# Performance work log

Hardware: AMD Instinct MI355X
Metric: run time of the kernel (lower is better)

## Reference

```python
import jax, jax.numpy as jnp
import numpy as np


def setup_inputs() -> dict:
    key = jax.random.key(0)
    ks = jax.random.split(key, 6)
    B, S, D, L = 4, 4096, 1024, 8192
    return {
        "inputs": jax.random.normal(ks[0], (B, S, D), dtype=jnp.float32),
        "W_w": jax.random.normal(ks[1], (D, D), dtype=jnp.float32) * (1.0 / np.sqrt(D)),
        "W_b": jax.random.normal(ks[2], (D,), dtype=jnp.float32) * 0.02,
        "U_w": jax.random.normal(ks[3], (L, D), dtype=jnp.float32) * (1.0 / np.sqrt(D)),
        "final_w": jax.random.normal(ks[4], (L, D), dtype=jnp.float32) * (1.0 / np.sqrt(D)),
        "final_b": jax.random.normal(ks[5], (L,), dtype=jnp.float32) * 0.02,
    }


def reference(inputs, W_w, W_b, U_w, final_w, final_b):
    # Z = tanh(W(inputs)): [B,S,D]
    Z = jnp.tanh(jnp.einsum("bsd,ed->bse", inputs, W_w) + W_b)
    # scores = U.weight @ Z^T: [B,L,S], softmax over seq
    scores = jnp.einsum("ld,bsd->bls", U_w, Z)
    alpha = jax.nn.softmax(scores, axis=2)
    # hidden = alpha @ inputs: [B,L,D]
    hidden = jnp.einsum("bls,bsd->bld", alpha, inputs)
    # logits = sum_d final_w[l,d]*hidden[b,l,d] + final_b[l]: [B,L]
    logits = jnp.einsum("ld,bld->bl", final_w, hidden) + final_b
    return logits
```

## Files before the change

### kernel.cpp

```cpp
#include <hip/hip_runtime.h>

typedef __attribute__((ext_vector_type(8))) short bf16x8;
typedef __attribute__((ext_vector_type(4))) float f32x4;

#define DEVINL __device__ __forceinline__
#define AS1 __attribute__((address_space(1)))
#define AS3 __attribute__((address_space(3)))

constexpr int BB = 4, SS = 4096, DD = 1024, LL = 8192;
constexpr int LT = 128, ST = 128, BK = 64, NS = 2;
constexpr int NL = LL / LT;
constexpr int SCHUNK = SS / NS;
constexpr int NST = SCHUNK / ST;
constexpr int KST = DD / BK;
constexpr int TILE = LT * BK;

DEVINL unsigned short f2bf(float f){
  union { float f; unsigned u; } a; a.f = f;
  unsigned r = a.u + 0x7fffu + ((a.u >> 16) & 1u);
  return (unsigned short)(r >> 16);
}

DEVINL void gll16(const void* src, void* dst){
  __builtin_amdgcn_global_load_lds((const AS1 unsigned int*)src,
                                   (AS3 unsigned int*)dst, 16, 0, 0);
}

DEVINL void stage_tile(const unsigned short* __restrict__ g0, int row0, int d0,
                       unsigned short* ldsbase, int wave, int lane){
#pragma unroll
  for (int it = 0; it < 4; ++it){
    int off  = it*4096 + wave*1024 + lane*16;
    int row  = off >> 7;
    int slot = (off >> 4) & 7;
    int scol = (slot ^ (row & 7)) << 3;
    gll16(g0 + (size_t)(row0 + row) * DD + d0 + scol,
          ldsbase + ((it*4096 + wave*1024) >> 1));
  }
}

DEVINL bf16x8 read_frag(const unsigned short* tile, int row, int chunk){
  return *(const AS3 bf16x8*)(tile + row*BK + ((chunk ^ (row & 7)) << 3));
}

__global__ void conv_kernel(const float4* __restrict__ in,
                            ushort4* __restrict__ out, int n4){
  int stride = gridDim.x * blockDim.x;
  for (int i = blockIdx.x*blockDim.x + threadIdx.x; i < n4; i += stride){
    float4 v = in[i];
    ushort4 o;
    o.x = f2bf(v.x); o.y = f2bf(v.y); o.z = f2bf(v.z); o.w = f2bf(v.w);
    out[i] = o;
  }
}

__global__ __launch_bounds__(256, 2) void zgemm_kernel(
    const unsigned short* __restrict__ X, const unsigned short* __restrict__ W,
    const float* __restrict__ Wb, unsigned short* __restrict__ Z)
{
  __shared__ __align__(16) unsigned short lds[2*TILE];
  const int bid = blockIdx.x;
  const int tm = bid & 127;
  const int tn = bid >> 7;
  const int tid = threadIdx.x, wave = tid >> 6, lane = tid & 63;
  const int wl = wave >> 1, wn = wave & 1;
  const int g = lane >> 4, cc = lane & 15;

  f32x4 acc[4][4] = {};
#pragma unroll 1
  for (int ks = 0; ks < KST; ++ks){
    __syncthreads();
    stage_tile(X, tm*LT, ks*BK, lds,        wave, lane);
    stage_tile(W, tn*LT, ks*BK, lds + TILE, wave, lane);
    __syncthreads();
#pragma unroll
    for (int ksub = 0; ksub < 2; ++ksub){
      bf16x8 af[4], bfr[4];
#pragma unroll
      for (int f = 0; f < 4; ++f) af[f]  = read_frag(lds,        wl*64 + f*16 + cc, ksub*4 + g);
#pragma unroll
      for (int f = 0; f < 4; ++f) bfr[f] = read_frag(lds + TILE, wn*64 + f*16 + cc, ksub*4 + g);
#pragma unroll
      for (int fm = 0; fm < 4; ++fm)
#pragma unroll
        for (int fn = 0; fn < 4; ++fn)
          acc[fm][fn] = __builtin_amdgcn_mfma_f32_16x16x32_bf16(af[fm], bfr[fn], acc[fm][fn], 0, 0, 0);
    }
  }
#pragma unroll
  for (int fm = 0; fm < 4; ++fm)
#pragma unroll
    for (int fn = 0; fn < 4; ++fn)
#pragma unroll
      for (int r = 0; r < 4; ++r){
        int row = tm*LT + wl*64 + fm*16 + 4*g + r;
        int col = tn*LT + wn*64 + fn*16 + cc;
        float y = acc[fm][fn][r] + Wb[col];
        float e2 = __expf(2.f * y);
        float t = 1.f - 2.f / (e2 + 1.f);
        Z[(size_t)row*DD + col] = f2bf(t);
      }
}

__global__ __launch_bounds__(256, 2) void fused_kernel(
    const unsigned short* __restrict__ U, const unsigned short* __restrict__ F,
    const unsigned short* __restrict__ Z, const unsigned short* __restrict__ X,
    float* __restrict__ pse, float* __restrict__ pac)
{
  __shared__ __align__(16) unsigned short lds[4*TILE];
  const int h = blockIdx.x;
  const int logical = (h & 7) * 64 + (h >> 3);
  const int lt  = logical & (NL - 1);
  const int grp = logical >> 6;
  const int sp  = grp & (NS - 1);
  const int b   = grp >> 1;

  const int tid = threadIdx.x, wave = tid >> 6, lane = tid & 63;
  const int wl = wave >> 1, wsc = wave & 1;
  const int g = lane >> 4, cc = lane & 15;

  const unsigned short* Ub = U + (size_t)lt*LT*DD;
  const unsigned short* Fb = F + (size_t)lt*LT*DD;
  const unsigned short* Zb = Z + ((size_t)b*SS + (size_t)sp*SCHUNK) * DD;
  const unsigned short* Xb = X + ((size_t)b*SS + (size_t)sp*SCHUNK) * DD;

  float se_st[4][4] = {}, ac_st[4][4] = {};

#pragma unroll 1
  for (int st = 0; st < NST; ++st){
    f32x4 sacc[4][4] = {}, gacc[4][4] = {};
#pragma unroll 1
    for (int ks = 0; ks < KST; ++ks){
      __syncthreads();
      stage_tile(Ub, 0,     ks*BK, lds,          wave, lane);
      stage_tile(Fb, 0,     ks*BK, lds +   TILE, wave, lane);
      stage_tile(Zb, st*ST, ks*BK, lds + 2*TILE, wave, lane);
      stage_tile(Xb, st*ST, ks*BK, lds + 3*TILE, wave, lane);
      __syncthreads();
#pragma unroll
      for (int ksub = 0; ksub < 2; ++ksub){
        bf16x8 a0[4], b0[4];
#pragma unroll
        for (int f = 0; f < 4; ++f) a0[f] = read_frag(lds,          wl*64  + f*16 + cc, ksub*4 + g);
#pragma unroll
        for (int f = 0; f < 4; ++f) b0[f] = read_frag(lds + 2*TILE, wsc*64 + f*16 + cc, ksub*4 + g);
#pragma unroll
        for (int fm = 0; fm < 4; ++fm)
#pragma unroll
          for (int fn = 0; fn < 4; ++fn)
            sacc[fm][fn] = __builtin_amdgcn_mfma_f32_16x16x32_bf16(a0[fm], b0[fn], sacc[fm][fn], 0, 0, 0);
#pragma unroll
        for (int f = 0; f < 4; ++f) a0[f] = read_frag(lds +   TILE, wl*64  + f*16 + cc, ksub*4 + g);
#pragma unroll
        for (int f = 0; f < 4; ++f) b0[f] = read_frag(lds + 3*TILE, wsc*64 + f*16 + cc, ksub*4 + g);
#pragma unroll
        for (int fm = 0; fm < 4; ++fm)
#pragma unroll
          for (int fn = 0; fn < 4; ++fn)
            gacc[fm][fn] = __builtin_amdgcn_mfma_f32_16x16x32_bf16(a0[fm], b0[fn], gacc[fm][fn], 0, 0, 0);
      }
    }
#pragma unroll
    for (int fm = 0; fm < 4; ++fm)
#pragma unroll
      for (int r = 0; r < 4; ++r){
        float ps = 0.f, pg = 0.f;
#pragma unroll
        for (int fn = 0; fn < 4; ++fn){
          float p = __expf(sacc[fm][fn][r]);
          ps += p;
          pg += p * gacc[fm][fn][r];
        }
        se_st[fm][r] += ps;
        ac_st[fm][r] += pg;
      }
  }
#pragma unroll
  for (int fm = 0; fm < 4; ++fm)
#pragma unroll
    for (int r = 0; r < 4; ++r){
      float s = se_st[fm][r], a = ac_st[fm][r];
#pragma unroll
      for (int m = 1; m < 16; m <<= 1){
        s += __shfl_xor(s, m, 64);
        a += __shfl_xor(a, m, 64);
      }
      if (cc == 0){
        int l = lt*LT + wl*64 + fm*16 + 4*g + r;
        size_t idx = ((((size_t)b*LL + l)*NS + sp) << 1) + wsc;
        pse[idx] = s;
        pac[idx] = a;
      }
    }
}

__global__ void combine_kernel(const float* __restrict__ pse, const float* __restrict__ pac,
                               const float* __restrict__ fb, float* __restrict__ out)
{
  int i = blockIdx.x*blockDim.x + threadIdx.x;
  if (i >= BB*LL) return;
  int l = i & (LL - 1);
  float s = 0.f, a = 0.f;
#pragma unroll
  for (int k = 0; k < NS*2; ++k){
    s += pse[(size_t)i*(NS*2) + k];
    a += pac[(size_t)i*(NS*2) + k];
  }
  out[i] = a / s + fb[l];
}

extern "C" void kernel_launch(void* const* d_in, const int* in_sizes, int n_in,
                              void* d_out, int out_size, void* d_ws, size_t ws_size,
                              hipStream_t stream)
{
  const float* inp = (const float*)d_in[0];
  const float* Ww  = (const float*)d_in[1];
  const float* Wb  = (const float*)d_in[2];
  const float* Uw  = (const float*)d_in[3];
  const float* Fw  = (const float*)d_in[4];
  const float* fb  = (const float*)d_in[5];
  float* out = (float*)d_out;

  char* ws = (char*)d_ws;
  unsigned short* Xbf = (unsigned short*)(ws);
  unsigned short* Zbf = (unsigned short*)(ws + (size_t)32*1024*1024);
  unsigned short* Ubf = (unsigned short*)(ws + (size_t)64*1024*1024);
  unsigned short* Fbf = (unsigned short*)(ws + (size_t)80*1024*1024);
  unsigned short* Wbf = (unsigned short*)(ws + (size_t)96*1024*1024);
  float* pse = (float*)(ws + (size_t)98*1024*1024);
  float* pac = (float*)(ws + (size_t)99*1024*1024);

  conv_kernel<<<2048, 256, 0, stream>>>((const float4*)inp, (ushort4*)Xbf, BB*SS*DD/4);
  conv_kernel<<<256,  256, 0, stream>>>((const float4*)Ww,  (ushort4*)Wbf, DD*DD/4);
  conv_kernel<<<1024, 256, 0, stream>>>((const float4*)Uw,  (ushort4*)Ubf, LL*DD/4);
  conv_kernel<<<1024, 256, 0, stream>>>((const float4*)Fw,  (ushort4*)Fbf, LL*DD/4);

  zgemm_kernel<<<128*8, 256, 0, stream>>>(Xbf, Wbf, Wb, Zbf);
  fused_kernel<<<BB*NL*NS, 256, 0, stream>>>(Ubf, Fbf, Zbf, Xbf, pse, pac);
  combine_kernel<<<(BB*LL + 255)/256, 256, 0, stream>>>(pse, pac, fb, out);
}
```

Measured before the change: 721.4 us.

## Triple-buffer fused attention GEMM with async LDS pipeline and larger L tile

The fused scores/values kernel is restructured into a single software-pipelined loop over work units. Each unit is one (S-tile, phase, k-step) where the phase selects either F·X or U·Z, and units are staged through a 3-slot LDS ring using direct global-to-LDS loads with a manual vmcnt wait. Blocks now use 512 threads and a 256-row L tile, so each Z/X tile is reused across twice as many L rows. The intent is to overlap global loads with MFMA work and cut redundant Z/X traffic. The cost is about 147KB of LDS per block and only 256 blocks, which limits occupancy to one block per CU. The wrap-around prefetch also issues a couple of redundant loads at the end.

```diff
diff --git a/kernel.cpp b/kernel.cpp
--- a/kernel.cpp
+++ b/kernel.cpp
@@ -8,12 +8,14 @@
 #define AS3 __attribute__((address_space(3)))
 
 constexpr int BB = 4, SS = 4096, DD = 1024, LL = 8192;
-constexpr int LT = 128, ST = 128, BK = 64, NS = 2;
-constexpr int NL = LL / LT;
-constexpr int SCHUNK = SS / NS;
-constexpr int NST = SCHUNK / ST;
+constexpr int NS = 2, SCHUNK = SS / NS;
+constexpr int LTILE = 256, STILE = 128, BK = 64;
+constexpr int NST = SCHUNK / STILE;
 constexpr int KST = DD / BK;
-constexpr int TILE = LT * BK;
+constexpr int NU  = NST * 2 * KST;
+constexpr int A_SH = LTILE * BK;
+constexpr int B_SH = STILE * BK;
+constexpr int SLOT_SH = A_SH + B_SH;
 
 DEVINL unsigned short f2bf(float f){
   union { float f; unsigned u; } a; a.f = f;
@@ -24,19 +26,6 @@
 DEVINL void gll16(const void* src, void* dst){
   __builtin_amdgcn_global_load_lds((const AS1 unsigned int*)src,
                                    (AS3 unsigned int*)dst, 16, 0, 0);
-}
-
-DEVINL void stage_tile(const unsigned short* __restrict__ g0, int row0, int d0,
-                       unsigned short* ldsbase, int wave, int lane){
-#pragma unroll
-  for (int it = 0; it < 4; ++it){
-    int off  = it*4096 + wave*1024 + lane*16;
-    int row  = off >> 7;
-    int slot = (off >> 4) & 7;
-    int scol = (slot ^ (row & 7)) << 3;
-    gll16(g0 + (size_t)(row0 + row) * DD + d0 + scol,
-          ldsbase + ((it*4096 + wave*1024) >> 1));
-  }
 }
 
 DEVINL bf16x8 read_frag(const unsigned short* tile, int row, int chunk){
@@ -54,11 +43,26 @@
   }
 }
 
+constexpr int ZTILE = 128 * BK;
+
+DEVINL void stage_tile128(const unsigned short* __restrict__ g0, int row0, int d0,
+                          unsigned short* ldsbase, int wave, int lane){
+#pragma unroll
+  for (int it = 0; it < 4; ++it){
+    int off  = it*4096 + wave*1024 + lane*16;
+    int row  = off >> 7;
+    int slot = (off >> 4) & 7;
+    int scol = (slot ^ (row & 7)) << 3;
+    gll16(g0 + (size_t)(row0 + row) * DD + d0 + scol,
+          ldsbase + ((it*4096 + wave*1024) >> 1));
+  }
+}
+
 __global__ __launch_bounds__(256, 2) void zgemm_kernel(
     const unsigned short* __restrict__ X, const unsigned short* __restrict__ W,
     const float* __restrict__ Wb, unsigned short* __restrict__ Z)
 {
-  __shared__ __align__(16) unsigned short lds[2*TILE];
+  __shared__ __align__(16) unsigned short lds[2*ZTILE];
   const int bid = blockIdx.x;
   const int tm = bid & 127;
   const int tn = bid >> 7;
@@ -70,16 +74,16 @@
 #pragma unroll 1
   for (int ks = 0; ks < KST; ++ks){
     __syncthreads();
-    stage_tile(X, tm*LT, ks*BK, lds,        wave, lane);
-    stage_tile(W, tn*LT, ks*BK, lds + TILE, wave, lane);
+    stage_tile128(X, tm*128, ks*BK, lds,         wave, lane);
+    stage_tile128(W, tn*128, ks*BK, lds + ZTILE, wave, lane);
     __syncthreads();
 #pragma unroll
     for (int ksub = 0; ksub < 2; ++ksub){
       bf16x8 af[4], bfr[4];
 #pragma unroll
-      for (int f = 0; f < 4; ++f) af[f]  = read_frag(lds,        wl*64 + f*16 + cc, ksub*4 + g);
-#pragma unroll
-      for (int f = 0; f < 4; ++f) bfr[f] = read_frag(lds + TILE, wn*64 + f*16 + cc, ksub*4 + g);
+      for (int f = 0; f < 4; ++f) af[f]  = read_frag(lds,         wl*64 + f*16 + cc, ksub*4 + g);
+#pragma unroll
+      for (int f = 0; f < 4; ++f) bfr[f] = read_frag(lds + ZTILE, wn*64 + f*16 + cc, ksub*4 + g);
 #pragma unroll
       for (int fm = 0; fm < 4; ++fm)
 #pragma unroll
@@ -93,8 +97,8 @@
     for (int fn = 0; fn < 4; ++fn)
 #pragma unroll
       for (int r = 0; r < 4; ++r){
-        int row = tm*LT + wl*64 + fm*16 + 4*g + r;
-        int col = tn*LT + wn*64 + fn*16 + cc;
+        int row = tm*128 + wl*64 + fm*16 + 4*g + r;
+        int col = tn*128 + wn*64 + fn*16 + cc;
         float y = acc[fm][fn][r] + Wb[col];
         float e2 = __expf(2.f * y);
         float t = 1.f - 2.f / (e2 + 1.f);
@@ -102,79 +106,122 @@
       }
 }
 
-__global__ __launch_bounds__(256, 2) void fused_kernel(
+DEVINL void stage_unit(int u, int slot,
+                       const unsigned short* Ub, const unsigned short* Fb,
+                       const unsigned short* Zb, const unsigned short* Xb,
+                       unsigned short* lds, int tid,
+                       const int* aoff, const int* boff)
+{
+  const int st = u >> 5, ph = (u >> 4) & 1, k64 = (u & 15) * 64;
+  const unsigned short* As = ph ? Ub : Fb;
+  const unsigned short* Bs = (ph ? Zb : Xb) + (size_t)st * (STILE * DD);
+  unsigned short* sl = lds + slot * SLOT_SH;
+#pragma unroll
+  for (int it = 0; it < 4; ++it)
+    gll16(As + aoff[it] + k64, sl + (it*512 + tid)*8);
+#pragma unroll
+  for (int it = 0; it < 2; ++it)
+    gll16(Bs + boff[it] + k64, sl + A_SH + (it*512 + tid)*8);
+}
+
+__global__ __launch_bounds__(512, 2) void fused_kernel(
     const unsigned short* __restrict__ U, const unsigned short* __restrict__ F,
     const unsigned short* __restrict__ Z, const unsigned short* __restrict__ X,
     float* __restrict__ pse, float* __restrict__ pac)
 {
-  __shared__ __align__(16) unsigned short lds[4*TILE];
+  __shared__ __align__(16) unsigned short lds[3 * SLOT_SH];
+
   const int h = blockIdx.x;
-  const int logical = (h & 7) * 64 + (h >> 3);
-  const int lt  = logical & (NL - 1);
-  const int grp = logical >> 6;
-  const int sp  = grp & (NS - 1);
-  const int b   = grp >> 1;
-
-  const int tid = threadIdx.x, wave = tid >> 6, lane = tid & 63;
-  const int wl = wave >> 1, wsc = wave & 1;
+  const int lt = h >> 3, grp = h & 7;
+  const int b = grp >> 1, sp = grp & 1;
+
+  const int tid = threadIdx.x;
+  const int wave = tid >> 6, lane = tid & 63;
+  const int wl = wave >> 1, ws = wave & 1;
   const int g = lane >> 4, cc = lane & 15;
 
-  const unsigned short* Ub = U + (size_t)lt*LT*DD;
-  const unsigned short* Fb = F + (size_t)lt*LT*DD;
-  const unsigned short* Zb = Z + ((size_t)b*SS + (size_t)sp*SCHUNK) * DD;
-  const unsigned short* Xb = X + ((size_t)b*SS + (size_t)sp*SCHUNK) * DD;
-
+  const unsigned short* Ub = U + (size_t)lt * LTILE * DD;
+  const unsigned short* Fb = F + (size_t)lt * LTILE * DD;
+  const unsigned short* Zb = Z + ((size_t)b * SS + (size_t)sp * SCHUNK) * DD;
+  const unsigned short* Xb = X + ((size_t)b * SS + (size_t)sp * SCHUNK) * DD;
+
+  int aoff[4], boff[2];
+#pragma unroll
+  for (int it = 0; it < 4; ++it){
+    int c = it*512 + tid, row = c >> 3, s0 = c & 7;
+    aoff[it] = row*DD + ((s0 ^ (row & 7)) << 3);
+  }
+#pragma unroll
+  for (int it = 0; it < 2; ++it){
+    int c = it*512 + tid, row = c >> 3, s0 = c & 7;
+    boff[it] = row*DD + ((s0 ^ (row & 7)) << 3);
+  }
+
+  f32x4 sacc[4][4] = {}, gacc[4][4] = {};
   float se_st[4][4] = {}, ac_st[4][4] = {};
 
+  stage_unit(0, 0, Ub, Fb, Zb, Xb, lds, tid, aoff, boff);
+  stage_unit(1, 1, Ub, Fb, Zb, Xb, lds, tid, aoff, boff);
+
 #pragma unroll 1
-  for (int st = 0; st < NST; ++st){
-    f32x4 sacc[4][4] = {}, gacc[4][4] = {};
-#pragma unroll 1
-    for (int ks = 0; ks < KST; ++ks){
-      __syncthreads();
-      stage_tile(Ub, 0,     ks*BK, lds,          wave, lane);
-      stage_tile(Fb, 0,     ks*BK, lds +   TILE, wave, lane);
-      stage_tile(Zb, st*ST, ks*BK, lds + 2*TILE, wave, lane);
-      stage_tile(Xb, st*ST, ks*BK, lds + 3*TILE, wave, lane);
-      __syncthreads();
-#pragma unroll
-      for (int ksub = 0; ksub < 2; ++ksub){
-        bf16x8 a0[4], b0[4];
-#pragma unroll
-        for (int f = 0; f < 4; ++f) a0[f] = read_frag(lds,          wl*64  + f*16 + cc, ksub*4 + g);
-#pragma unroll
-        for (int f = 0; f < 4; ++f) b0[f] = read_frag(lds + 2*TILE, wsc*64 + f*16 + cc, ksub*4 + g);
+  for (int u = 0; u < NU; ++u){
+    asm volatile("s_waitcnt vmcnt(6)" ::: "memory");
+    __builtin_amdgcn_s_barrier();
+
+    int un = u + 2; if (un >= NU) un -= NU;
+    stage_unit(un, (u + 2) % 3, Ub, Fb, Zb, Xb, lds, tid, aoff, boff);
+
+    const unsigned short* At = lds + (u % 3) * SLOT_SH;
+    const unsigned short* Bt = At + A_SH;
+    const int ph = (u >> 4) & 1;
+
+#pragma unroll
+    for (int ksub = 0; ksub < 2; ++ksub){
+      bf16x8 a0[4], b0[4];
+#pragma unroll
+      for (int f = 0; f < 4; ++f) a0[f] = read_frag(At, wl*64 + f*16 + cc, ksub*4 + g);
+#pragma unroll
+      for (int f = 0; f < 4; ++f) b0[f] = read_frag(Bt, ws*64 + f*16 + cc, ksub*4 + g);
+      if (ph == 0){
+#pragma unroll
+        for (int fm = 0; fm < 4; ++fm)
+#pragma unroll
+          for (int fn = 0; fn < 4; ++fn)
+            gacc[fm][fn] = __builtin_amdgcn_mfma_f32_16x16x32_bf16(a0[fm], b0[fn], gacc[fm][fn], 0, 0, 0);
+      } else {
 #pragma unroll
         for (int fm = 0; fm < 4; ++fm)
 #pragma unroll
           for (int fn = 0; fn < 4; ++fn)
             sacc[fm][fn] = __builtin_amdgcn_mfma_f32_16x16x32_bf16(a0[fm], b0[fn], sacc[fm][fn], 0, 0, 0);
-#pragma unroll
-        for (int f = 0; f < 4; ++f) a0[f] = read_frag(lds +   TILE, wl*64  + f*16 + cc, ksub*4 + g);
-#pragma unroll
-        for (int f = 0; f < 4; ++f) b0[f] = read_frag(lds + 3*TILE, wsc*64 + f*16 + cc, ksub*4 + g);
-#pragma unroll
-        for (int fm = 0; fm < 4; ++fm)
-#pragma unroll
-          for (int fn = 0; fn < 4; ++fn)
-            gacc[fm][fn] = __builtin_amdgcn_mfma_f32_16x16x32_bf16(a0[fm], b0[fn], gacc[fm][fn], 0, 0, 0);
-      }
-    }
-#pragma unroll
-    for (int fm = 0; fm < 4; ++fm)
-#pragma unroll
-      for (int r = 0; r < 4; ++r){
-        float ps = 0.f, pg = 0.f;
+      }
+    }
+
+    if ((u & 31) == 31){
+#pragma unroll
+      for (int fm = 0; fm < 4; ++fm)
+#pragma unroll
+        for (int r = 0; r < 4; ++r){
+          float ps = 0.f, pg = 0.f;
+#pragma unroll
+          for (int fn = 0; fn < 4; ++fn){
+            float p = __expf(sacc[fm][fn][r]);
+            ps += p;
+            pg += p * gacc[fm][fn][r];
+          }
+          se_st[fm][r] += ps;
+          ac_st[fm][r] += pg;
+        }
+#pragma unroll
+      for (int fm = 0; fm < 4; ++fm)
 #pragma unroll
         for (int fn = 0; fn < 4; ++fn){
-          float p = __expf(sacc[fm][fn][r]);
-          ps += p;
-          pg += p * gacc[fm][fn][r];
+          sacc[fm][fn] = f32x4{0.f, 0.f, 0.f, 0.f};
+          gacc[fm][fn] = f32x4{0.f, 0.f, 0.f, 0.f};
         }
-        se_st[fm][r] += ps;
-        ac_st[fm][r] += pg;
-      }
-  }
+    }
+  }
+
 #pragma unroll
   for (int fm = 0; fm < 4; ++fm)
 #pragma unroll
@@ -186,8 +233,8 @@
         a += __shfl_xor(a, m, 64);
       }
       if (cc == 0){
-        int l = lt*LT + wl*64 + fm*16 + 4*g + r;
-        size_t idx = ((((size_t)b*LL + l)*NS + sp) << 1) + wsc;
+        int l = lt*LTILE + wl*64 + fm*16 + 4*g + r;
+        size_t idx = ((((size_t)b*LL + l)*NS + sp) << 1) + ws;
         pse[idx] = s;
         pac[idx] = a;
       }
@@ -236,6 +283,6 @@
   conv_kernel<<<1024, 256, 0, stream>>>((const float4*)Fw,  (ushort4*)Fbf, LL*DD/4);
 
   zgemm_kernel<<<128*8, 256, 0, stream>>>(Xbf, Wbf, Wb, Zbf);
-  fused_kernel<<<BB*NL*NS, 256, 0, stream>>>(Ubf, Fbf, Zbf, Xbf, pse, pac);
+  fused_kernel<<<256, 512, 0, stream>>>(Ubf, Fbf, Zbf, Xbf, pse, pac);
   combine_kernel<<<(BB*LL + 255)/256, 256, 0, stream>>>(pse, pac, fb, out);
 }
```

Result: slower. 842.3 us (+16.8%).
